# Kernel optimization log

Hardware: AMD Instinct MI355X
Metric: run time of the kernel (lower is better)

Reference implementation:

```python
import jax, jax.numpy as jnp
import numpy as np

N, D_IN, H, D_EMB = 2048, 128, 256, 64


def setup_inputs() -> dict:
    key = jax.random.key(0)
    ks = jax.random.split(key, 8)
    x = jax.random.normal(ks[0], (N, D_IN), dtype=jnp.float32)
    adj = jnp.zeros((N, N), dtype=jnp.float32)  # only its last dim is used (eye sizing)
    s = 0.05
    W0 = jax.random.normal(ks[1], (D_IN, H), dtype=jnp.float32) * s
    b0 = jnp.zeros((H,), dtype=jnp.float32)
    W1 = jax.random.normal(ks[2], (H, D_EMB), dtype=jnp.float32) * s
    b1 = jnp.zeros((D_EMB,), dtype=jnp.float32)
    W2 = jax.random.normal(ks[3], (D_IN, D_IN), dtype=jnp.float32) * s
    b2 = jnp.zeros((D_IN,), dtype=jnp.float32)
    temp = jnp.float32(0.1)
    theta = jnp.float32(0.1)
    return {"x": x, "adj": adj, "W0": W0, "b0": b0, "W1": W1, "b1": b1,
            "W2": W2, "b2": b2, "temp": temp, "theta": theta}


def reference(x, adj, W0, b0, W1, b1, W2, b2, temp, theta):
    # layer 0 (on x) and middle layer 1 (on out_x), both with ReLU activation
    out_x = jax.nn.relu(x @ W0 + b0)            # [N, H]
    emb = jax.nn.relu(out_x @ W1 + b1)          # [N, D_EMB]
    # last layer is applied to the ORIGINAL x (per the `x = model(x)` branch)
    x_last = x @ W2 + b2                        # [N, D_IN]

    # dist[i,j] = -||emb_i - emb_j||^2, computed via the gemm expansion
    sq = jnp.sum(emb * emb, axis=1)             # [N]
    dist = -(sq[:, None] + sq[None, :] - 2.0 * (emb @ emb.T))  # [N, N]

    prob = jax.nn.sigmoid((1.0 + temp) * dist + (5.0 + theta))
    A = prob + jnp.eye(adj.shape[-1], dtype=prob.dtype)        # [N, N]

    # diag(A.sum(-1))^{-1} @ A @ x_last  ==  rowwise divide by degree
    deg = jnp.sum(A, axis=-1)                   # [N]
    out = jax.nn.relu((A @ x_last) / deg[:, None])

    # sigmoid(.) > 0 everywhere, so all N*N entries are nonzero: adj_wts is the
    # full flattened adjacency (data-independent shape, jit-safe)
    adj_wts = A.reshape(-1)
    return out, adj_wts
```

## Files before the change

### kernel.cpp

```cpp
#include <hip/hip_runtime.h>
#include <hip/hip_bf16.h>


typedef short bf16x8 __attribute__((ext_vector_type(8)));
typedef float f32x4 __attribute__((ext_vector_type(4)));

__device__ __forceinline__ unsigned short f2bf(float f) {
    unsigned u = __float_as_uint(f);
    unsigned r = u + 0x7fffu + ((u >> 16) & 1u);
    return (unsigned short)(r >> 16);
}

__device__ __forceinline__ bf16x8 pack_rne8(const float* p) {
    union { unsigned u[4]; bf16x8 v; } r;
    #pragma unroll
    for (int i = 0; i < 4; ++i) {
        unsigned lo = __float_as_uint(p[2 * i]) + 0x8000u;
        unsigned hi = __float_as_uint(p[2 * i + 1]) + 0x8000u;
        r.u[i] = __builtin_amdgcn_perm(hi, lo, 0x07060302u);
    }
    return r.v;
}

__device__ __forceinline__ bf16x8 pack_bf8(const float* p) {
    union { unsigned u[4]; bf16x8 v; } r;
    #pragma unroll
    for (int i = 0; i < 4; ++i)
        r.u[i] = __builtin_amdgcn_perm(__float_as_uint(p[2 * i + 1]),
                                       __float_as_uint(p[2 * i]), 0x07060302u);
    return r.v;
}

__global__ __launch_bounds__(256, 2) void k1_mfma(
    const float* __restrict__ x,
    const float* __restrict__ W0, const float* __restrict__ b0,
    const float* __restrict__ W1, const float* __restrict__ b1,
    const float* __restrict__ W2, const float* __restrict__ b2,
    unsigned short* __restrict__ emb_bf,
    unsigned short* __restrict__ xlT_bf,
    float* __restrict__ sq)
{
    constexpr int LDO = 264;
    __shared__ unsigned short oxb[16 * LDO];
    __shared__ float sqs[4][16];

    const int t = threadIdx.x;
    const int lane = t & 63;
    const int w = t >> 6;
    const int m = lane & 15;
    const int q = lane >> 4;
    const int tile = blockIdx.x >> 1;
    const int role = blockIdx.x & 1;
    const int i0 = tile * 16;

    bf16x8 ax[4];
    #pragma unroll
    for (int kb = 0; kb < 4; ++kb) {
        float xf[8];
        *(f32x4*)&xf[0] = *(const f32x4*)(x + (size_t)(i0 + m) * 128 + kb * 32 + q * 8);
        *(f32x4*)&xf[4] = *(const f32x4*)(x + (size_t)(i0 + m) * 128 + kb * 32 + q * 8 + 4);
        ax[kb] = pack_rne8(xf);
    }

    if (role == 0) {
        const int h1 = w * 16 + m;
        const float bias1 = b1[h1];
        bf16x8 wp[8];
        #pragma unroll
        for (int kb = 0; kb < 8; ++kb) {
            float wf[8];
            #pragma unroll
            for (int j = 0; j < 8; ++j) wf[j] = W1[(size_t)(kb * 32 + q * 8 + j) * 64 + h1];
            wp[kb] = pack_rne8(wf);
        }

        #pragma unroll
        for (int hh = 0; hh < 4; ++hh) {
            const int h = (w * 4 + hh) * 16 + m;
            float bb = b0[h];
            f32x4 acc = {bb, bb, bb, bb};
            #pragma unroll
            for (int kb = 0; kb < 4; ++kb) {
                float wf[8];
                #pragma unroll
                for (int j = 0; j < 8; ++j) wf[j] = W0[(size_t)(kb * 32 + q * 8 + j) * 256 + h];
                acc = __builtin_amdgcn_mfma_f32_16x16x32_bf16(ax[kb], pack_rne8(wf), acc, 0, 0, 0);
            }
            #pragma unroll
            for (int r = 0; r < 4; ++r)
                oxb[(q * 4 + r) * LDO + h] = f2bf(fmaxf(acc[r], 0.0f));
        }
        __syncthreads();

        f32x4 acc = {bias1, bias1, bias1, bias1};
        #pragma unroll
        for (int kb = 0; kb < 8; ++kb) {
            bf16x8 af = *(const bf16x8*)(&oxb[m * LDO + kb * 32 + q * 8]);
            acc = __builtin_amdgcn_mfma_f32_16x16x32_bf16(af, wp[kb], acc, 0, 0, 0);
        }
        float s2[4];
        #pragma unroll
        for (int r = 0; r < 4; ++r) {
            float e = fmaxf(acc[r], 0.0f);
            emb_bf[(size_t)(i0 + q * 4 + r) * 64 + h1] = f2bf(e);
            s2[r] = e * e;
        }
        #pragma unroll
        for (int r = 0; r < 4; ++r) {
            float v = s2[r];
            v += __shfl_xor(v, 1);
            v += __shfl_xor(v, 2);
            v += __shfl_xor(v, 4);
            v += __shfl_xor(v, 8);
            if (m == 0) sqs[w][q * 4 + r] = v;
        }
        __syncthreads();
        if (t < 16)
            sq[i0 + t] = sqs[0][t] + sqs[1][t] + sqs[2][t] + sqs[3][t];
    } else {
        bf16x8 wp[8];
        #pragma unroll
        for (int hh = 0; hh < 2; ++hh) {
            const int c = (w * 2 + hh) * 16 + m;
            #pragma unroll
            for (int kb = 0; kb < 4; ++kb) {
                float wf[8];
                #pragma unroll
                for (int j = 0; j < 8; ++j) wf[j] = W2[(size_t)(kb * 32 + q * 8 + j) * 128 + c];
                wp[hh * 4 + kb] = pack_rne8(wf);
            }
        }
        #pragma unroll
        for (int hh = 0; hh < 2; ++hh) {
            const int c = (w * 2 + hh) * 16 + m;
            float bb = b2[c];
            f32x4 acc = {bb, bb, bb, bb};
            #pragma unroll
            for (int kb = 0; kb < 4; ++kb)
                acc = __builtin_amdgcn_mfma_f32_16x16x32_bf16(ax[kb], wp[hh * 4 + kb], acc, 0, 0, 0);
            uint2 pk;
            pk.x = (unsigned)f2bf(acc[0]) | ((unsigned)f2bf(acc[1]) << 16);
            pk.y = (unsigned)f2bf(acc[2]) | ((unsigned)f2bf(acc[3]) << 16);
            *(uint2*)(&xlT_bf[(size_t)c * 2048 + i0 + q * 4]) = pk;
        }
    }
}

__global__ __launch_bounds__(512, 4) void k2h(
    const unsigned short* __restrict__ emb_bf,
    const unsigned short* __restrict__ xlT_bf,
    const float* __restrict__ sq,
    const float* __restrict__ tempp, const float* __restrict__ thetap,
    float* __restrict__ adjw,
    float* __restrict__ outPart,
    float* __restrict__ degPart)
{
    constexpr int LDP = 132;
    __shared__ float Pt[2][16 * LDP];
    __shared__ float degS[8][16];

    const int t = threadIdx.x;
    const int lane = t & 63;
    const int w = t >> 6;
    const int m = lane & 15;
    const int q = lane >> 4;
    const int i0 = blockIdx.x * 16;
    const int half = blockIdx.y;
    const int jbase = half * 1024;
    const float scale = 1.0f + tempp[0];
    const float bias = 5.0f + thetap[0];

    bf16x8 a0 = *(const bf16x8*)(emb_bf + (size_t)(i0 + m) * 64 + q * 8);
    bf16x8 a1 = *(const bf16x8*)(emb_bf + (size_t)(i0 + m) * 64 + 32 + q * 8);
    float sqIr[4];
    #pragma unroll
    for (int r = 0; r < 4; ++r) sqIr[r] = sq[i0 + q * 4 + r];

    f32x4 accO = {0.f, 0.f, 0.f, 0.f};
    float dega[4] = {0.f, 0.f, 0.f, 0.f};
    const int cg = w * 16;

    for (int jt = 0; jt < 8; ++jt) {
        const int j0 = jbase + jt * 128;
        float* P = &Pt[jt & 1][0];

        bf16x8 xb[4];
        #pragma unroll
        for (int s = 0; s < 4; ++s)
            xb[s] = *(const bf16x8*)(xlT_bf + (size_t)(cg + m) * 2048 + j0 + s * 32 + q * 8);

        {
            const int col = w * 16 + m;
            const int gcol = j0 + col;
            const unsigned short* ebj = emb_bf + (size_t)gcol * 64;
            bf16x8 b0 = *(const bf16x8*)(ebj + q * 8);
            bf16x8 b1 = *(const bf16x8*)(ebj + 32 + q * 8);
            f32x4 S = {0.f, 0.f, 0.f, 0.f};
            S = __builtin_amdgcn_mfma_f32_16x16x32_bf16(a0, b0, S, 0, 0, 0);
            S = __builtin_amdgcn_mfma_f32_16x16x32_bf16(a1, b1, S, 0, 0, 0);

            const float csqJ = sq[gcol];
            #pragma unroll
            for (int r = 0; r < 4; ++r) {
                int grow = i0 + q * 4 + r;
                float dist = 2.0f * S[r] - sqIr[r] - csqJ;
                float z = scale * dist + bias;
                float p = __builtin_amdgcn_rcpf(1.0f + __expf(-z));
                if (grow == gcol) p += 1.0f;
                dega[r] += p;
                P[(q * 4 + r) * LDP + col] = p;
            }
        }
        __syncthreads();

        {
            int row = t >> 5;
            int c0 = (t & 31) * 4;
            f32x4 v = *(const f32x4*)(&P[row * LDP + c0]);
            *(f32x4*)(adjw + (size_t)(i0 + row) * 2048 + j0 + c0) = v;
        }

        #pragma unroll
        for (int s = 0; s < 4; ++s) {
            float af[8];
            *(f32x4*)(&af[0]) = *(const f32x4*)(&P[m * LDP + s * 32 + q * 8]);
            *(f32x4*)(&af[4]) = *(const f32x4*)(&P[m * LDP + s * 32 + q * 8 + 4]);
            bf16x8 aa = pack_bf8(af);
            accO = __builtin_amdgcn_mfma_f32_16x16x32_bf16(aa, xb[s], accO, 0, 0, 0);
        }
    }

    #pragma unroll
    for (int r = 0; r < 4; ++r) {
        float v = dega[r];
        v += __shfl_xor(v, 1);
        v += __shfl_xor(v, 2);
        v += __shfl_xor(v, 4);
        v += __shfl_xor(v, 8);
        if (m == 0) degS[w][q * 4 + r] = v;
    }
    __syncthreads();
    if (t < 16) {
        float d = 0.f;
        #pragma unroll
        for (int ww = 0; ww < 8; ++ww) d += degS[ww][t];
        degPart[half * 2048 + i0 + t] = d;
    }

    float* op = outPart + (size_t)half * 262144 + (size_t)i0 * 128 + cg + m;
    #pragma unroll
    for (int r = 0; r < 4; ++r)
        op[(size_t)(q * 4 + r) * 128] = accO[r];
}

__global__ __launch_bounds__(256) void k3_fin(
    const float* __restrict__ outPart, const float* __restrict__ degPart,
    float* __restrict__ out)
{
    int gid = blockIdx.x * 256 + threadIdx.x;
    int i = gid >> 5;
    int c0 = (gid & 31) * 4;
    f32x4 v0 = *(const f32x4*)(outPart + (size_t)i * 128 + c0);
    f32x4 v1 = *(const f32x4*)(outPart + 262144 + (size_t)i * 128 + c0);
    float dinv = 1.0f / (degPart[i] + degPart[2048 + i]);
    f32x4 o;
    #pragma unroll
    for (int r = 0; r < 4; ++r) o[r] = fmaxf((v0[r] + v1[r]) * dinv, 0.f);
    *(f32x4*)(out + (size_t)i * 128 + c0) = o;
}

extern "C" void kernel_launch(void* const* d_in, const int* in_sizes, int n_in,
                              void* d_out, int out_size, void* d_ws, size_t ws_size,
                              hipStream_t stream) {
    (void)in_sizes; (void)n_in; (void)out_size; (void)ws_size;
    const float* x     = (const float*)d_in[0];
    const float* W0    = (const float*)d_in[2];
    const float* b0    = (const float*)d_in[3];
    const float* W1    = (const float*)d_in[4];
    const float* b1    = (const float*)d_in[5];
    const float* W2    = (const float*)d_in[6];
    const float* b2    = (const float*)d_in[7];
    const float* temp  = (const float*)d_in[8];
    const float* theta = (const float*)d_in[9];

    char* ws = (char*)d_ws;
    unsigned short* emb_bf = (unsigned short*)(ws);
    unsigned short* xlT_bf = (unsigned short*)(ws + 262144);
    float* sq      = (float*)(ws + 786432);
    float* degPart = (float*)(ws + 794624);
    float* outPart = (float*)(ws + 811008);

    float* out  = (float*)d_out;
    float* adjw = (float*)d_out + 262144;

    k1_mfma<<<256, 256, 0, stream>>>(x, W0, b0, W1, b1, W2, b2,
                                     emb_bf, xlT_bf, sq);
    k2h<<<dim3(128, 2), 512, 0, stream>>>(emb_bf, xlT_bf, sq, temp, theta,
                                          adjw, outPart, degPart);
    k3_fin<<<256, 256, 0, stream>>>(outPart, degPart, out);
}
```

Before: 108.0 us.

## Use 8-row blocks over full j range and fuse final normalization

Instead of splitting the j dimension into two halves with partial out/deg buffers and a separate finishing kernel, each block now handles 8 rows over all 2048 columns. The degree normalization and ReLU are done in the same kernel. This removes a kernel launch and the partial-sum round trip through global memory while keeping 256 blocks. The cost is that half of each MFMA tile goes unused (rows duplicated via m&7, only q<2 lanes compute the sigmoid), so MFMA and S-computation efficiency per output row drops.

```diff
diff --git a/kernel.cpp b/kernel.cpp
--- a/kernel.cpp
+++ b/kernel.cpp
@@ -146,42 +146,41 @@
     }
 }
 
-__global__ __launch_bounds__(512, 4) void k2h(
+__global__ __launch_bounds__(512, 2) void k2full(
     const unsigned short* __restrict__ emb_bf,
     const unsigned short* __restrict__ xlT_bf,
     const float* __restrict__ sq,
     const float* __restrict__ tempp, const float* __restrict__ thetap,
     float* __restrict__ adjw,
-    float* __restrict__ outPart,
-    float* __restrict__ degPart)
+    float* __restrict__ out)
 {
     constexpr int LDP = 132;
-    __shared__ float Pt[2][16 * LDP];
-    __shared__ float degS[8][16];
+    __shared__ float Pt[2][8 * LDP];
+    __shared__ float degS[8][8];
+    __shared__ float degF[8];
 
     const int t = threadIdx.x;
     const int lane = t & 63;
     const int w = t >> 6;
     const int m = lane & 15;
     const int q = lane >> 4;
-    const int i0 = blockIdx.x * 16;
-    const int half = blockIdx.y;
-    const int jbase = half * 1024;
+    const int i0 = blockIdx.x * 8;
     const float scale = 1.0f + tempp[0];
     const float bias = 5.0f + thetap[0];
 
-    bf16x8 a0 = *(const bf16x8*)(emb_bf + (size_t)(i0 + m) * 64 + q * 8);
-    bf16x8 a1 = *(const bf16x8*)(emb_bf + (size_t)(i0 + m) * 64 + 32 + q * 8);
+    const int arow = i0 + (m & 7);
+    bf16x8 a0 = *(const bf16x8*)(emb_bf + (size_t)arow * 64 + q * 8);
+    bf16x8 a1 = *(const bf16x8*)(emb_bf + (size_t)arow * 64 + 32 + q * 8);
     float sqIr[4];
     #pragma unroll
-    for (int r = 0; r < 4; ++r) sqIr[r] = sq[i0 + q * 4 + r];
+    for (int r = 0; r < 4; ++r) sqIr[r] = sq[i0 + ((q * 4 + r) & 7)];
 
     f32x4 accO = {0.f, 0.f, 0.f, 0.f};
     float dega[4] = {0.f, 0.f, 0.f, 0.f};
     const int cg = w * 16;
 
-    for (int jt = 0; jt < 8; ++jt) {
-        const int j0 = jbase + jt * 128;
+    for (int jt = 0; jt < 16; ++jt) {
+        const int j0 = jt * 128;
         float* P = &Pt[jt & 1][0];
 
         bf16x8 xb[4];
@@ -200,31 +199,33 @@
             S = __builtin_amdgcn_mfma_f32_16x16x32_bf16(a1, b1, S, 0, 0, 0);
 
             const float csqJ = sq[gcol];
-            #pragma unroll
-            for (int r = 0; r < 4; ++r) {
-                int grow = i0 + q * 4 + r;
-                float dist = 2.0f * S[r] - sqIr[r] - csqJ;
-                float z = scale * dist + bias;
-                float p = __builtin_amdgcn_rcpf(1.0f + __expf(-z));
-                if (grow == gcol) p += 1.0f;
-                dega[r] += p;
-                P[(q * 4 + r) * LDP + col] = p;
+            if (q < 2) {
+                #pragma unroll
+                for (int r = 0; r < 4; ++r) {
+                    int grow = i0 + q * 4 + r;
+                    float dist = 2.0f * S[r] - sqIr[r] - csqJ;
+                    float z = scale * dist + bias;
+                    float p = __builtin_amdgcn_rcpf(1.0f + __expf(-z));
+                    if (grow == gcol) p += 1.0f;
+                    dega[r] += p;
+                    P[(q * 4 + r) * LDP + col] = p;
+                }
             }
         }
         __syncthreads();
 
         {
-            int row = t >> 5;
-            int c0 = (t & 31) * 4;
-            f32x4 v = *(const f32x4*)(&P[row * LDP + c0]);
-            *(f32x4*)(adjw + (size_t)(i0 + row) * 2048 + j0 + c0) = v;
+            int row = t >> 6;
+            int c = t & 63;
+            float2 v = *(const float2*)(&P[row * LDP + c * 2]);
+            *(float2*)(adjw + (size_t)(i0 + row) * 2048 + j0 + c * 2) = v;
         }
 
         #pragma unroll
         for (int s = 0; s < 4; ++s) {
             float af[8];
-            *(f32x4*)(&af[0]) = *(const f32x4*)(&P[m * LDP + s * 32 + q * 8]);
-            *(f32x4*)(&af[4]) = *(const f32x4*)(&P[m * LDP + s * 32 + q * 8 + 4]);
+            *(f32x4*)(&af[0]) = *(const f32x4*)(&P[(m & 7) * LDP + s * 32 + q * 8]);
+            *(f32x4*)(&af[4]) = *(const f32x4*)(&P[(m & 7) * LDP + s * 32 + q * 8 + 4]);
             bf16x8 aa = pack_bf8(af);
             accO = __builtin_amdgcn_mfma_f32_16x16x32_bf16(aa, xb[s], accO, 0, 0, 0);
         }
@@ -237,36 +238,24 @@
         v += __shfl_xor(v, 2);
         v += __shfl_xor(v, 4);
         v += __shfl_xor(v, 8);
-        if (m == 0) degS[w][q * 4 + r] = v;
+        if (m == 0 && q < 2) degS[w][q * 4 + r] = v;
     }
     __syncthreads();
-    if (t < 16) {
+    if (t < 8) {
         float d = 0.f;
         #pragma unroll
         for (int ww = 0; ww < 8; ++ww) d += degS[ww][t];
-        degPart[half * 2048 + i0 + t] = d;
-    }
-
-    float* op = outPart + (size_t)half * 262144 + (size_t)i0 * 128 + cg + m;
-    #pragma unroll
-    for (int r = 0; r < 4; ++r)
-        op[(size_t)(q * 4 + r) * 128] = accO[r];
-}
-
-__global__ __launch_bounds__(256) void k3_fin(
-    const float* __restrict__ outPart, const float* __restrict__ degPart,
-    float* __restrict__ out)
-{
-    int gid = blockIdx.x * 256 + threadIdx.x;
-    int i = gid >> 5;
-    int c0 = (gid & 31) * 4;
-    f32x4 v0 = *(const f32x4*)(outPart + (size_t)i * 128 + c0);
-    f32x4 v1 = *(const f32x4*)(outPart + 262144 + (size_t)i * 128 + c0);
-    float dinv = 1.0f / (degPart[i] + degPart[2048 + i]);
-    f32x4 o;
-    #pragma unroll
-    for (int r = 0; r < 4; ++r) o[r] = fmaxf((v0[r] + v1[r]) * dinv, 0.f);
-    *(f32x4*)(out + (size_t)i * 128 + c0) = o;
+        degF[t] = d;
+    }
+    __syncthreads();
+
+    if (q < 2) {
+        #pragma unroll
+        for (int r = 0; r < 4; ++r) {
+            float dinv = 1.0f / degF[q * 4 + r];
+            out[(size_t)(i0 + q * 4 + r) * 128 + cg + m] = fmaxf(accO[r] * dinv, 0.f);
+        }
+    }
 }
 
 extern "C" void kernel_launch(void* const* d_in, const int* in_sizes, int n_in,
@@ -287,15 +276,12 @@
     unsigned short* emb_bf = (unsigned short*)(ws);
     unsigned short* xlT_bf = (unsigned short*)(ws + 262144);
     float* sq      = (float*)(ws + 786432);
-    float* degPart = (float*)(ws + 794624);
-    float* outPart = (float*)(ws + 811008);
 
     float* out  = (float*)d_out;
     float* adjw = (float*)d_out + 262144;
 
     k1_mfma<<<256, 256, 0, stream>>>(x, W0, b0, W1, b1, W2, b2,
                                      emb_bf, xlT_bf, sq);
-    k2h<<<dim3(128, 2), 512, 0, stream>>>(emb_bf, xlT_bf, sq, temp, theta,
-                                          adjw, outPart, degPart);
-    k3_fin<<<256, 256, 0, stream>>>(outPart, degPart, out);
-}
+    k2full<<<256, 512, 0, stream>>>(emb_bf, xlT_bf, sq, temp, theta,
+                                    adjw, out);
+}
```

Result: slower. 126.4 us (+17.1%).
